# Optimization experiments

Hardware: AMD Instinct MI355X
Metric: run time of the kernel (lower is better)

## Reference

```python
import jax, jax.numpy as jnp
import numpy as np

N_NODE = 50000
N_EDGE = 800000
NODE_DIM, EDGE_DIM = 3, 4


def _relu(x):
    return jnp.maximum(x, 0)


def setup_inputs() -> dict:
    key = jax.random.key(0)
    ks = jax.random.split(key, 32)
    ki = iter(range(32))

    def w(shape):
        fan = shape[0]
        return (jax.random.normal(ks[next(ki)], shape, jnp.float32) / np.float32(np.sqrt(fan)))

    def b(n):
        return jnp.zeros((n,), jnp.float32)

    inp = {
        'nodes': jax.random.normal(ks[next(ki)], (N_NODE, NODE_DIM), jnp.float32),
        'edges': jax.random.normal(ks[next(ki)], (N_EDGE, EDGE_DIM), jnp.float32),
        'senders': jax.random.randint(ks[next(ki)], (N_EDGE,), 0, N_NODE, jnp.int32),
        'receivers': jax.random.randint(ks[next(ki)], (N_EDGE,), 0, N_NODE, jnp.int32),
        # psi1 encoder: [10 -> 256 -> 256 -> 128], relu after every layer (act_final=True)
        'mw0': w((NODE_DIM * 2 + EDGE_DIM, 256)), 'mb0': b(256),
        'mw1': w((256, 256)), 'mb1': b(256),
        'mw2': w((256, 128)), 'mb2': b(128),
        # psi2 attention: [128 -> 128 -> 128 -> 1], no final act
        'aw0': w((128, 128)), 'ab0': b(128),
        'aw1': w((128, 128)), 'ab1': b(128),
        'aw2': w((128, 1)), 'ab2': b(1),
        # psi3 value: [128 -> 256 -> 128], relu after every layer
        'vw0': w((128, 256)), 'vb0': b(256),
        'vw1': w((256, 128)), 'vb1': b(128),
        # psi4 decoder: [128 -> 256 -> 256 -> 1], no final act
        'uw0': w((128, 256)), 'ub0': b(256),
        'uw1': w((256, 256)), 'ub1': b(256),
        'uw2': w((256, 1)), 'ub2': b(1),
    }
    return inp


def reference(nodes, edges, senders, receivers,
              mw0, mb0, mw1, mb1, mw2, mb2,
              aw0, ab0, aw1, ab1, aw2, ab2,
              vw0, vb0, vw1, vb1,
              uw0, ub0, uw1, ub1, uw2, ub2):
    n_node = nodes.shape[0]
    # gather endpoint features and concat with edge features: (E, 2*node_dim+edge_dim)
    z = jnp.concatenate([nodes[senders], nodes[receivers], edges], axis=-1)
    # psi1 encoder (act_final=True)
    q = _relu(_relu(_relu(z @ mw0 + mb0) @ mw1 + mb1) @ mw2 + mb2)  # (E,128)
    # psi2 attention logits (no final act)
    w = (_relu(_relu(q @ aw0 + ab0) @ aw1 + ab1) @ aw2 + ab2)[:, 0]  # (E,)
    # segment softmax over receivers (matches torch scatter_reduce amax with -1e9 init)
    m = jax.ops.segment_max(w, receivers, num_segments=n_node)
    m = jnp.maximum(m, jnp.float32(-1e9))
    ex = jnp.exp(w - m[receivers])
    s = jax.ops.segment_sum(ex, receivers, num_segments=n_node)
    attn = ex / (s[receivers] + 1e-12)  # (E,)
    # psi3 value (act_final=True)
    v = _relu(_relu(q @ vw0 + vb0) @ vw1 + vb1)  # (E,128)
    # attention-weighted scatter-add aggregation to receiver nodes
    aggr = jax.ops.segment_sum(attn[:, None] * v, receivers, num_segments=n_node)  # (N,128)
    # psi4 decoder (no final act)
    out = _relu(_relu(aggr @ uw0 + ub0) @ uw1 + ub1) @ uw2 + ub2  # (N,1)
    return out
```

## Files before the change

kernel.cpp:

```cpp
#include <hip/hip_runtime.h>
#include <stdint.h>

#define NN_NODE 50000
#define NN_EDGE 800000

typedef _Float16 f16;
typedef _Float16 f16x2 __attribute__((ext_vector_type(2)));
typedef _Float16 f16x4 __attribute__((ext_vector_type(4)));
typedef _Float16 f16x8 __attribute__((ext_vector_type(8)));
typedef float f32x4 __attribute__((ext_vector_type(4)));

#define WT_MW0   0
#define WT_MW1   8192
#define WT_MW2   73728
#define WT_AW0   106496
#define WT_AW1   122880
#define WT_VW0   139264
#define WT_VW1   172032
#define WT_UW0   204800
#define WT_UW1   237568
#define WT_TOTAL 303104

#define V_OFF      606208ull
#define WL_OFF     205406208ull
#define CNT_OFF    208606208ull
#define BASE_OFF   208806208ull
#define AGGR_OFF   209006208ull

__device__ __forceinline__ int swz(int row, int col) {
    return row * 256 + ((((col >> 3) ^ (row & 7))) << 3) + (col & 7);
}

template<int K, int N, int NKN, int EPI>
__device__ __forceinline__ void mlayer(const f16* in, int inoff,
        const f16* __restrict__ wt, const float* __restrict__ bias,
        f16* out, int outoff,
        f16x8* bf0, const f16* __restrict__ wtn, f16x8* bfn,
        const float* __restrict__ aw2, float* lpart,
        f16* __restrict__ vout, const int* sposp, int tid)
{
    const int wave = tid >> 6;
    const int lane = tid & 63;
    const int l15  = lane & 15;
    const int quad = lane >> 4;
    constexpr int NKS = K >> 5;
    constexpr int NCT = N >> 4;
    constexpr int ITC = NCT / 4;

    f16x8 af[4][NKS];
#pragma unroll
    for (int ms = 0; ms < 4; ++ms)
#pragma unroll
        for (int ks = 0; ks < NKS; ++ks)
            af[ms][ks] = *(const f16x8*)(in + swz(ms * 16 + l15, inoff + ks * 32 + quad * 8));

    if constexpr (NKN > 0) {
        const f16* wrow = wtn + (size_t)(wave * 16 + l15) * (NKN * 32) + quad * 8;
#pragma unroll
        for (int ks = 0; ks < NKN; ++ks) bfn[ks] = *(const f16x8*)(wrow + ks * 32);
    }

    int   sposv[4];
    float preg[4];
    if constexpr (EPI == 2) {
#pragma unroll
        for (int ms = 0; ms < 4; ++ms) sposv[ms] = sposp[ms * 16 + l15];
    }
    if constexpr (EPI == 1) {
#pragma unroll
        for (int ms = 0; ms < 4; ++ms) preg[ms] = 0.f;
    }

    f16x8 bfl[2][NKS > 0 ? NKS : 1];
#pragma unroll
    for (int ks = 0; ks < NKS; ++ks) bfl[0][ks] = bf0[ks];

#pragma unroll
    for (int i = 0; i < ITC; ++i) {
        const int ct = wave + i * 4;
        if (i + 1 < ITC) {
            const f16* wrow = wt + (size_t)((ct + 4) * 16 + l15) * K + quad * 8;
#pragma unroll
            for (int ks = 0; ks < NKS; ++ks)
                bfl[(i + 1) & 1][ks] = *(const f16x8*)(wrow + ks * 32);
        }
        const int f0 = ct * 16 + quad * 4;
        const float4 bv = *(const float4*)(bias + f0);
        float4 awv;
        if constexpr (EPI == 1) awv = *(const float4*)(aw2 + f0);
#pragma unroll
        for (int ms = 0; ms < 4; ++ms) {
            f32x4 acc = {0.f, 0.f, 0.f, 0.f};
#pragma unroll
            for (int ks = 0; ks < NKS; ++ks)
                acc = __builtin_amdgcn_mfma_f32_16x16x32_f16(bfl[i & 1][ks], af[ms][ks], acc, 0, 0, 0);
            if constexpr (EPI == 0) {
                f16x4 o;
                o[0] = (f16)fmaxf(acc[0] + bv.x, 0.f);
                o[1] = (f16)fmaxf(acc[1] + bv.y, 0.f);
                o[2] = (f16)fmaxf(acc[2] + bv.z, 0.f);
                o[3] = (f16)fmaxf(acc[3] + bv.w, 0.f);
                *(f16x4*)(out + swz(ms * 16 + l15, outoff + f0)) = o;
            } else if constexpr (EPI == 1) {
                preg[ms] += fmaxf(acc[0] + bv.x, 0.f) * awv.x
                          + fmaxf(acc[1] + bv.y, 0.f) * awv.y
                          + fmaxf(acc[2] + bv.z, 0.f) * awv.z
                          + fmaxf(acc[3] + bv.w, 0.f) * awv.w;
            } else {
                f16x4 o;
                o[0] = (f16)fmaxf(acc[0] + bv.x, 0.f);
                o[1] = (f16)fmaxf(acc[1] + bv.y, 0.f);
                o[2] = (f16)fmaxf(acc[2] + bv.z, 0.f);
                o[3] = (f16)fmaxf(acc[3] + bv.w, 0.f);
                *(f16x4*)(vout + (size_t)sposv[ms] * 128 + f0) = o;
            }
        }
    }
    if constexpr (EPI == 1) {
#pragma unroll
        for (int ms = 0; ms < 4; ++ms) {
            float r = preg[ms];
            r += __shfl_xor(r, 16);
            r += __shfl_xor(r, 32);
            if (quad == 0) lpart[wave * 64 + ms * 16 + l15] = r;
        }
    }
}

template<int K, int N>
__device__ __forceinline__ void mfma_layer_basic(const f16* in, int inoff,
        const f16* __restrict__ wt, const float* __restrict__ bias,
        f16* out, int outoff, int tid)
{
    const int wave = tid >> 6;
    const int lane = tid & 63;
    const int l15  = lane & 15;
    const int quad = lane >> 4;
    constexpr int NCT = N >> 4;
    constexpr int NKS = K >> 5;
    f16x8 af[4][NKS];
#pragma unroll
    for (int ms = 0; ms < 4; ++ms)
#pragma unroll
        for (int ks = 0; ks < NKS; ++ks)
            af[ms][ks] = *(const f16x8*)(in + swz(ms * 16 + l15, inoff + ks * 32 + quad * 8));
#pragma unroll 1
    for (int ct = wave; ct < NCT; ct += 4) {
        f16x8 bf[NKS];
        const f16* wrow = wt + (size_t)(ct * 16 + l15) * K + quad * 8;
#pragma unroll
        for (int ks = 0; ks < NKS; ++ks) bf[ks] = *(const f16x8*)(wrow + ks * 32);
        const int f0 = ct * 16 + quad * 4;
        const float4 bv = *(const float4*)(bias + f0);
#pragma unroll
        for (int ms = 0; ms < 4; ++ms) {
            f32x4 acc = {0.f, 0.f, 0.f, 0.f};
#pragma unroll
            for (int ks = 0; ks < NKS; ++ks)
                acc = __builtin_amdgcn_mfma_f32_16x16x32_f16(bf[ks], af[ms][ks], acc, 0, 0, 0);
            f16x4 o;
            o[0] = (f16)fmaxf(acc[0] + bv.x, 0.f);
            o[1] = (f16)fmaxf(acc[1] + bv.y, 0.f);
            o[2] = (f16)fmaxf(acc[2] + bv.z, 0.f);
            o[3] = (f16)fmaxf(acc[3] + bv.w, 0.f);
            *(f16x4*)(out + swz(ms * 16 + l15, outoff + f0)) = o;
        }
    }
}

struct WSeg { const float* src; int K, N, Kpad, dstOff; };
struct WSegs { WSeg s[9]; };

__global__ void prep_kernel(WSegs segs, f16* __restrict__ wt) {
    int idx = blockIdx.x * 256 + threadIdx.x;
    if (idx >= WT_TOTAL) return;
    int off = idx;
#pragma unroll
    for (int i = 0; i < 9; ++i) {
        int sz = segs.s[i].N * segs.s[i].Kpad;
        if (off < sz) {
            int n = off / segs.s[i].Kpad;
            int k = off - n * segs.s[i].Kpad;
            f16 val = (f16)0.f;
            if (k < segs.s[i].K) val = (f16)segs.s[i].src[k * segs.s[i].N + n];
            wt[segs.s[i].dstOff + off] = val;
            return;
        }
        off -= sz;
    }
}

__global__ void hist_kernel(const int* __restrict__ receivers, int* __restrict__ cnt) {
    int e = blockIdx.x * 256 + threadIdx.x;
    atomicAdd(&cnt[receivers[e]], 1);
}

__global__ __launch_bounds__(1024) void scan_kernel(int* __restrict__ cnt, int* __restrict__ base) {
    __shared__ int psum[1024];
    const int tid = threadIdx.x;
    const int CH = (NN_NODE + 1023) / 1024;
    const int lo = tid * CH;
    const int hi = min(lo + CH, NN_NODE);
    int s = 0;
    for (int i = lo; i < hi; ++i) s += cnt[i];
    psum[tid] = s;
    __syncthreads();
    for (int d = 1; d < 1024; d <<= 1) {
        int v = (tid >= d) ? psum[tid - d] : 0;
        __syncthreads();
        psum[tid] += v;
        __syncthreads();
    }
    int run = psum[tid] - s;
    for (int i = lo; i < hi; ++i) {
        int c = cnt[i];
        base[i] = run;
        cnt[i] = run;
        run += c;
    }
}

__global__ __launch_bounds__(256, 2) void edge_kernel(
        const float* __restrict__ nodes, const float* __restrict__ edges,
        const int* __restrict__ senders, const int* __restrict__ receivers,
        const f16* __restrict__ wt,
        const float* __restrict__ mb0, const float* __restrict__ mb1, const float* __restrict__ mb2,
        const float* __restrict__ ab0, const float* __restrict__ ab1,
        const float* __restrict__ aw2, const float* __restrict__ ab2,
        const float* __restrict__ vb0, const float* __restrict__ vb1,
        f16* __restrict__ vout, float* __restrict__ wlog, int* __restrict__ cursor)
{
    __shared__ f16 ldsbuf[2 * 64 * 256];
    __shared__ int spos[64];
    __shared__ float lpart[256];
    f16* bufA = ldsbuf;
    f16* bufB = ldsbuf + 64 * 256;
    const int tid = threadIdx.x;
    const int e0 = blockIdx.x * 64;
    const int wave = tid >> 6;
    const int lane = tid & 63;
    const int l15  = lane & 15;
    const int quad = lane >> 4;

    f16x8 bfA[8], bfB[8];

    {
        const f16* wrow = wt + WT_MW0 + (size_t)(wave * 16 + l15) * 32 + quad * 8;
        bfA[0] = *(const f16x8*)wrow;
    }

    {
        const int e = tid & 63, c = tid >> 6;
        f16x8 zv = {(f16)0.f,(f16)0.f,(f16)0.f,(f16)0.f,(f16)0.f,(f16)0.f,(f16)0.f,(f16)0.f};
        if (c == 0) {
            int s = senders[e0 + e];
            int r = receivers[e0 + e];
            const float2 ev = *(const float2*)(edges + (size_t)(e0 + e) * 4);
            zv[0] = (f16)nodes[s * 3 + 0]; zv[1] = (f16)nodes[s * 3 + 1]; zv[2] = (f16)nodes[s * 3 + 2];
            zv[3] = (f16)nodes[r * 3 + 0]; zv[4] = (f16)nodes[r * 3 + 1]; zv[5] = (f16)nodes[r * 3 + 2];
            zv[6] = (f16)ev.x; zv[7] = (f16)ev.y;
        } else if (c == 1) {
            const float2 ev = *(const float2*)(edges + (size_t)(e0 + e) * 4 + 2);
            zv[0] = (f16)ev.x; zv[1] = (f16)ev.y;
        }
        *(f16x8*)(bufA + e * 256 + ((c ^ (e & 7)) << 3)) = zv;
    }
    __syncthreads();

    mlayer< 32, 256, 8, 0>(bufA, 0, wt + WT_MW0, mb0, bufB, 0, bfA, wt + WT_MW1, bfB,
                           nullptr, nullptr, nullptr, nullptr, tid);
    __syncthreads();
    mlayer<256, 256, 8, 0>(bufB, 0, wt + WT_MW1, mb1, bufA, 0, bfB, wt + WT_MW2, bfA,
                           nullptr, nullptr, nullptr, nullptr, tid);
    __syncthreads();
    mlayer<256, 128, 4, 0>(bufA, 0, wt + WT_MW2, mb2, bufB, 0, bfA, wt + WT_AW0, bfB,
                           nullptr, nullptr, nullptr, nullptr, tid);
    __syncthreads();
    mlayer<128, 128, 4, 0>(bufB, 0, wt + WT_AW0, ab0, bufA, 0, bfB, wt + WT_AW1, bfA,
                           nullptr, nullptr, nullptr, nullptr, tid);
    __syncthreads();
    mlayer<128, 128, 4, 1>(bufA, 0, wt + WT_AW1, ab1, nullptr, 0, bfA, wt + WT_VW0, bfB,
                           aw2, lpart, nullptr, nullptr, tid);
    __syncthreads();

    if (tid < 64) {
        float wv = lpart[tid] + lpart[64 + tid] + lpart[128 + tid] + lpart[192 + tid] + ab2[0];
        int r = receivers[e0 + tid];
        int pos = atomicAdd(&cursor[r], 1);
        spos[tid] = pos;
        wlog[pos] = wv;
    }
    mlayer<128, 256, 8, 0>(bufB, 0, wt + WT_VW0, vb0, bufA, 0, bfB, wt + WT_VW1, bfA,
                           nullptr, nullptr, nullptr, nullptr, tid);
    __syncthreads();
    mlayer<256, 128, 0, 2>(bufA, 0, wt + WT_VW1, vb1, nullptr, 0, bfA, nullptr, nullptr,
                           nullptr, nullptr, vout, spos, tid);
}

__global__ __launch_bounds__(256) void aggregate_kernel(
        const float* __restrict__ wlog, const f16* __restrict__ v,
        const int* __restrict__ base, float* __restrict__ aggr)
{
    const int tid = threadIdx.x;
    const int n = blockIdx.x * 4 + (tid >> 6);
    const int lane = tid & 63;
    const int st = base[n];
    const int en = (n == NN_NODE - 1) ? NN_EDGE : base[n + 1];

    float mx = -1e9f;
    for (int i = st + lane; i < en; i += 64) mx = fmaxf(mx, wlog[i]);
#pragma unroll
    for (int d = 1; d < 64; d <<= 1) mx = fmaxf(mx, __shfl_xor(mx, d));

    float sm = 0.f;
    for (int i = st + lane; i < en; i += 64) sm += __expf(wlog[i] - mx);
#pragma unroll
    for (int d = 1; d < 64; d <<= 1) sm += __shfl_xor(sm, d);
    const float inv = 1.f / (sm + 1e-12f);

    float acc0 = 0.f, acc1 = 0.f;
    const f16* vp = v + (size_t)st * 128 + lane * 2;
    for (int i = st; i < en; ++i, vp += 128) {
        float attn = __expf(wlog[i] - mx) * inv;
        f16x2 vv = *(const f16x2*)vp;
        acc0 += attn * (float)vv[0];
        acc1 += attn * (float)vv[1];
    }
    float2 o; o.x = acc0; o.y = acc1;
    *(float2*)(aggr + (size_t)n * 128 + lane * 2) = o;
}

__global__ __launch_bounds__(256, 2) void node_kernel(
        const float* __restrict__ aggr, const f16* __restrict__ wt,
        const float* __restrict__ ub0, const float* __restrict__ ub1,
        const float* __restrict__ uw2, const float* __restrict__ ub2,
        float* __restrict__ out)
{
    __shared__ f16 ldsbuf[2 * 64 * 256];
    f16* bufA = ldsbuf;
    f16* bufB = ldsbuf + 64 * 256;
    const int tid = threadIdx.x;
    const int n0 = blockIdx.x * 64;
    {
        int row = tid >> 2, j = tid & 3;
        int n = n0 + row;
        if (n < NN_NODE) {
            const float4* src = (const float4*)(aggr + (size_t)n * 128 + j * 32);
#pragma unroll
            for (int i = 0; i < 8; ++i) {
                float4 t4 = src[i];
                int c = j * 32 + i * 4;
                bufA[swz(row, c + 0)] = (f16)t4.x;
                bufA[swz(row, c + 1)] = (f16)t4.y;
                bufA[swz(row, c + 2)] = (f16)t4.z;
                bufA[swz(row, c + 3)] = (f16)t4.w;
            }
        } else {
#pragma unroll
            for (int i = 0; i < 32; ++i) bufA[swz(row, j * 32 + i)] = (f16)0.f;
        }
    }
    __syncthreads();
    mfma_layer_basic<128, 256>(bufA, 0, wt + WT_UW0, ub0, bufB, 0, tid); __syncthreads();
    mfma_layer_basic<256, 256>(bufB, 0, wt + WT_UW1, ub1, bufA, 0, tid); __syncthreads();
    {
        int e = tid >> 2, part = tid & 3;
        float sum = 0.f;
        for (int c = part * 64; c < part * 64 + 64; ++c)
            sum += (float)bufA[swz(e, c)] * uw2[c];
        sum += __shfl_down(sum, 2);
        sum += __shfl_down(sum, 1);
        int n = n0 + e;
        if (part == 0 && n < NN_NODE) out[n] = sum + ub2[0];
    }
}

extern "C" void kernel_launch(void* const* d_in, const int* in_sizes, int n_in,
                              void* d_out, int out_size, void* d_ws, size_t ws_size,
                              hipStream_t stream)
{
    const float* nodes     = (const float*)d_in[0];
    const float* edges     = (const float*)d_in[1];
    const int*   senders   = (const int*)d_in[2];
    const int*   receivers = (const int*)d_in[3];
    const float* mw0 = (const float*)d_in[4];  const float* mb0 = (const float*)d_in[5];
    const float* mw1 = (const float*)d_in[6];  const float* mb1 = (const float*)d_in[7];
    const float* mw2 = (const float*)d_in[8];  const float* mb2 = (const float*)d_in[9];
    const float* aw0 = (const float*)d_in[10]; const float* ab0 = (const float*)d_in[11];
    const float* aw1 = (const float*)d_in[12]; const float* ab1 = (const float*)d_in[13];
    const float* aw2 = (const float*)d_in[14]; const float* ab2 = (const float*)d_in[15];
    const float* vw0 = (const float*)d_in[16]; const float* vb0 = (const float*)d_in[17];
    const float* vw1 = (const float*)d_in[18]; const float* vb1 = (const float*)d_in[19];
    const float* uw0 = (const float*)d_in[20]; const float* ub0 = (const float*)d_in[21];
    const float* uw1 = (const float*)d_in[22]; const float* ub1 = (const float*)d_in[23];
    const float* uw2 = (const float*)d_in[24]; const float* ub2 = (const float*)d_in[25];

    char* ws = (char*)d_ws;
    f16*   wt   = (f16*)ws;
    f16*   vbuf = (f16*)(ws + V_OFF);
    float* wlog = (float*)(ws + WL_OFF);
    int*   cnt  = (int*)(ws + CNT_OFF);
    int*   base = (int*)(ws + BASE_OFF);
    float* aggr = (float*)(ws + AGGR_OFF);
    float* out  = (float*)d_out;

    hipMemsetAsync(cnt, 0, NN_NODE * sizeof(int), stream);

    WSegs segs = {{
        { mw0,  10, 256,  32, WT_MW0 },
        { mw1, 256, 256, 256, WT_MW1 },
        { mw2, 256, 128, 256, WT_MW2 },
        { aw0, 128, 128, 128, WT_AW0 },
        { aw1, 128, 128, 128, WT_AW1 },
        { vw0, 128, 256, 128, WT_VW0 },
        { vw1, 256, 128, 256, WT_VW1 },
        { uw0, 128, 256, 128, WT_UW0 },
        { uw1, 256, 256, 256, WT_UW1 },
    }};
    prep_kernel<<<(WT_TOTAL + 255) / 256, 256, 0, stream>>>(segs, wt);

    hist_kernel<<<NN_EDGE / 256, 256, 0, stream>>>(receivers, cnt);
    scan_kernel<<<1, 1024, 0, stream>>>(cnt, base);

    edge_kernel<<<NN_EDGE / 64, 256, 0, stream>>>(nodes, edges, senders, receivers, wt,
        mb0, mb1, mb2, ab0, ab1, aw2, ab2, vb0, vb1, vbuf, wlog, cnt);

    aggregate_kernel<<<NN_NODE / 4, 256, 0, stream>>>(wlog, vbuf, base, aggr);

    node_kernel<<<(NN_NODE + 63) / 64, 256, 0, stream>>>(aggr, wt, ub0, ub1, uw2, ub2, out);
}
```

Baseline: 995.7 us.

## Widen edge and node kernels to 8 waves and fuse decoder final dot

Edge and node kernels now launch 512 threads (8 waves), each wave owning fewer column tiles per layer, with launch bounds requesting 4 blocks per CU. The node kernel now uses the pipelined mlayer path with a fused final uw2 dot-product epilogue and vectorized packed f16 conversion when loading aggr. Output conversions use the packed cvt_pkrtz instruction, and the aggregate kernel clamps its segment bounds. More waves per block aim to hide latency and spread the MFMA work, but the 64 KB of LDS per block may limit how many blocks can actually reside on a CU.

```diff
diff --git a/kernel.cpp b/kernel.cpp
--- a/kernel.cpp
+++ b/kernel.cpp
@@ -31,12 +31,16 @@
     return row * 256 + ((((col >> 3) ^ (row & 7))) << 3) + (col & 7);
 }
 
-template<int K, int N, int NKN, int EPI>
+__device__ __forceinline__ f16x2 pk2(float a, float b) {
+    return __builtin_bit_cast(f16x2, __builtin_amdgcn_cvt_pkrtz(a, b));
+}
+
+template<int K, int N, int NKN, int EPI, int NW>
 __device__ __forceinline__ void mlayer(const f16* in, int inoff,
         const f16* __restrict__ wt, const float* __restrict__ bias,
         f16* out, int outoff,
         f16x8* bf0, const f16* __restrict__ wtn, f16x8* bfn,
-        const float* __restrict__ aw2, float* lpart,
+        const float* __restrict__ dvec, float* lpart,
         f16* __restrict__ vout, const int* sposp, int tid)
 {
     const int wave = tid >> 6;
@@ -45,7 +49,7 @@
     const int quad = lane >> 4;
     constexpr int NKS = K >> 5;
     constexpr int NCT = N >> 4;
-    constexpr int ITC = NCT / 4;
+    constexpr int ITC = NCT / NW;
 
     f16x8 af[4][NKS];
 #pragma unroll
@@ -77,9 +81,9 @@
 
 #pragma unroll
     for (int i = 0; i < ITC; ++i) {
-        const int ct = wave + i * 4;
+        const int ct = wave + i * NW;
         if (i + 1 < ITC) {
-            const f16* wrow = wt + (size_t)((ct + 4) * 16 + l15) * K + quad * 8;
+            const f16* wrow = wt + (size_t)((ct + NW) * 16 + l15) * K + quad * 8;
 #pragma unroll
             for (int ks = 0; ks < NKS; ++ks)
                 bfl[(i + 1) & 1][ks] = *(const f16x8*)(wrow + ks * 32);
@@ -87,32 +91,26 @@
         const int f0 = ct * 16 + quad * 4;
         const float4 bv = *(const float4*)(bias + f0);
         float4 awv;
-        if constexpr (EPI == 1) awv = *(const float4*)(aw2 + f0);
+        if constexpr (EPI == 1) awv = *(const float4*)(dvec + f0);
 #pragma unroll
         for (int ms = 0; ms < 4; ++ms) {
             f32x4 acc = {0.f, 0.f, 0.f, 0.f};
 #pragma unroll
             for (int ks = 0; ks < NKS; ++ks)
                 acc = __builtin_amdgcn_mfma_f32_16x16x32_f16(bfl[i & 1][ks], af[ms][ks], acc, 0, 0, 0);
-            if constexpr (EPI == 0) {
-                f16x4 o;
-                o[0] = (f16)fmaxf(acc[0] + bv.x, 0.f);
-                o[1] = (f16)fmaxf(acc[1] + bv.y, 0.f);
-                o[2] = (f16)fmaxf(acc[2] + bv.z, 0.f);
-                o[3] = (f16)fmaxf(acc[3] + bv.w, 0.f);
-                *(f16x4*)(out + swz(ms * 16 + l15, outoff + f0)) = o;
-            } else if constexpr (EPI == 1) {
+            if constexpr (EPI == 1) {
                 preg[ms] += fmaxf(acc[0] + bv.x, 0.f) * awv.x
                           + fmaxf(acc[1] + bv.y, 0.f) * awv.y
                           + fmaxf(acc[2] + bv.z, 0.f) * awv.z
                           + fmaxf(acc[3] + bv.w, 0.f) * awv.w;
             } else {
-                f16x4 o;
-                o[0] = (f16)fmaxf(acc[0] + bv.x, 0.f);
-                o[1] = (f16)fmaxf(acc[1] + bv.y, 0.f);
-                o[2] = (f16)fmaxf(acc[2] + bv.z, 0.f);
-                o[3] = (f16)fmaxf(acc[3] + bv.w, 0.f);
-                *(f16x4*)(vout + (size_t)sposv[ms] * 128 + f0) = o;
+                f16x2 lo = pk2(fmaxf(acc[0] + bv.x, 0.f), fmaxf(acc[1] + bv.y, 0.f));
+                f16x2 hi = pk2(fmaxf(acc[2] + bv.z, 0.f), fmaxf(acc[3] + bv.w, 0.f));
+                f16x4 o; o[0] = lo[0]; o[1] = lo[1]; o[2] = hi[0]; o[3] = hi[1];
+                if constexpr (EPI == 0)
+                    *(f16x4*)(out + swz(ms * 16 + l15, outoff + f0)) = o;
+                else
+                    *(f16x4*)(vout + (size_t)sposv[ms] * 128 + f0) = o;
             }
         }
     }
@@ -123,47 +121,6 @@
             r += __shfl_xor(r, 16);
             r += __shfl_xor(r, 32);
             if (quad == 0) lpart[wave * 64 + ms * 16 + l15] = r;
-        }
-    }
-}
-
-template<int K, int N>
-__device__ __forceinline__ void mfma_layer_basic(const f16* in, int inoff,
-        const f16* __restrict__ wt, const float* __restrict__ bias,
-        f16* out, int outoff, int tid)
-{
-    const int wave = tid >> 6;
-    const int lane = tid & 63;
-    const int l15  = lane & 15;
-    const int quad = lane >> 4;
-    constexpr int NCT = N >> 4;
-    constexpr int NKS = K >> 5;
-    f16x8 af[4][NKS];
-#pragma unroll
-    for (int ms = 0; ms < 4; ++ms)
-#pragma unroll
-        for (int ks = 0; ks < NKS; ++ks)
-            af[ms][ks] = *(const f16x8*)(in + swz(ms * 16 + l15, inoff + ks * 32 + quad * 8));
-#pragma unroll 1
-    for (int ct = wave; ct < NCT; ct += 4) {
-        f16x8 bf[NKS];
-        const f16* wrow = wt + (size_t)(ct * 16 + l15) * K + quad * 8;
-#pragma unroll
-        for (int ks = 0; ks < NKS; ++ks) bf[ks] = *(const f16x8*)(wrow + ks * 32);
-        const int f0 = ct * 16 + quad * 4;
-        const float4 bv = *(const float4*)(bias + f0);
-#pragma unroll
-        for (int ms = 0; ms < 4; ++ms) {
-            f32x4 acc = {0.f, 0.f, 0.f, 0.f};
-#pragma unroll
-            for (int ks = 0; ks < NKS; ++ks)
-                acc = __builtin_amdgcn_mfma_f32_16x16x32_f16(bf[ks], af[ms][ks], acc, 0, 0, 0);
-            f16x4 o;
-            o[0] = (f16)fmaxf(acc[0] + bv.x, 0.f);
-            o[1] = (f16)fmaxf(acc[1] + bv.y, 0.f);
-            o[2] = (f16)fmaxf(acc[2] + bv.z, 0.f);
-            o[3] = (f16)fmaxf(acc[3] + bv.w, 0.f);
-            *(f16x4*)(out + swz(ms * 16 + l15, outoff + f0)) = o;
         }
     }
 }
@@ -220,7 +177,7 @@
     }
 }
 
-__global__ __launch_bounds__(256, 2) void edge_kernel(
+__global__ __launch_bounds__(512, 4) void edge_kernel(
         const float* __restrict__ nodes, const float* __restrict__ edges,
         const int* __restrict__ senders, const int* __restrict__ receivers,
         const f16* __restrict__ wt,
@@ -232,7 +189,7 @@
 {
     __shared__ f16 ldsbuf[2 * 64 * 256];
     __shared__ int spos[64];
-    __shared__ float lpart[256];
+    __shared__ float lpart[512];
     f16* bufA = ldsbuf;
     f16* bufB = ldsbuf + 64 * 256;
     const int tid = threadIdx.x;
@@ -251,50 +208,54 @@
 
     {
         const int e = tid & 63, c = tid >> 6;
-        f16x8 zv = {(f16)0.f,(f16)0.f,(f16)0.f,(f16)0.f,(f16)0.f,(f16)0.f,(f16)0.f,(f16)0.f};
-        if (c == 0) {
-            int s = senders[e0 + e];
-            int r = receivers[e0 + e];
-            const float2 ev = *(const float2*)(edges + (size_t)(e0 + e) * 4);
-            zv[0] = (f16)nodes[s * 3 + 0]; zv[1] = (f16)nodes[s * 3 + 1]; zv[2] = (f16)nodes[s * 3 + 2];
-            zv[3] = (f16)nodes[r * 3 + 0]; zv[4] = (f16)nodes[r * 3 + 1]; zv[5] = (f16)nodes[r * 3 + 2];
-            zv[6] = (f16)ev.x; zv[7] = (f16)ev.y;
-        } else if (c == 1) {
-            const float2 ev = *(const float2*)(edges + (size_t)(e0 + e) * 4 + 2);
-            zv[0] = (f16)ev.x; zv[1] = (f16)ev.y;
-        }
-        *(f16x8*)(bufA + e * 256 + ((c ^ (e & 7)) << 3)) = zv;
-    }
-    __syncthreads();
-
-    mlayer< 32, 256, 8, 0>(bufA, 0, wt + WT_MW0, mb0, bufB, 0, bfA, wt + WT_MW1, bfB,
-                           nullptr, nullptr, nullptr, nullptr, tid);
-    __syncthreads();
-    mlayer<256, 256, 8, 0>(bufB, 0, wt + WT_MW1, mb1, bufA, 0, bfB, wt + WT_MW2, bfA,
-                           nullptr, nullptr, nullptr, nullptr, tid);
-    __syncthreads();
-    mlayer<256, 128, 4, 0>(bufA, 0, wt + WT_MW2, mb2, bufB, 0, bfA, wt + WT_AW0, bfB,
-                           nullptr, nullptr, nullptr, nullptr, tid);
-    __syncthreads();
-    mlayer<128, 128, 4, 0>(bufB, 0, wt + WT_AW0, ab0, bufA, 0, bfB, wt + WT_AW1, bfA,
-                           nullptr, nullptr, nullptr, nullptr, tid);
-    __syncthreads();
-    mlayer<128, 128, 4, 1>(bufA, 0, wt + WT_AW1, ab1, nullptr, 0, bfA, wt + WT_VW0, bfB,
-                           aw2, lpart, nullptr, nullptr, tid);
+        if (c < 4) {
+            f16x8 zv = {(f16)0.f,(f16)0.f,(f16)0.f,(f16)0.f,(f16)0.f,(f16)0.f,(f16)0.f,(f16)0.f};
+            if (c == 0) {
+                int s = senders[e0 + e];
+                int r = receivers[e0 + e];
+                const float2 ev = *(const float2*)(edges + (size_t)(e0 + e) * 4);
+                zv[0] = (f16)nodes[s * 3 + 0]; zv[1] = (f16)nodes[s * 3 + 1]; zv[2] = (f16)nodes[s * 3 + 2];
+                zv[3] = (f16)nodes[r * 3 + 0]; zv[4] = (f16)nodes[r * 3 + 1]; zv[5] = (f16)nodes[r * 3 + 2];
+                zv[6] = (f16)ev.x; zv[7] = (f16)ev.y;
+            } else if (c == 1) {
+                const float2 ev = *(const float2*)(edges + (size_t)(e0 + e) * 4 + 2);
+                zv[0] = (f16)ev.x; zv[1] = (f16)ev.y;
+            }
+            *(f16x8*)(bufA + e * 256 + ((c ^ (e & 7)) << 3)) = zv;
+        }
+    }
+    __syncthreads();
+
+    mlayer< 32, 256, 8, 0, 8>(bufA, 0, wt + WT_MW0, mb0, bufB, 0, bfA, wt + WT_MW1, bfB,
+                              nullptr, nullptr, nullptr, nullptr, tid);
+    __syncthreads();
+    mlayer<256, 256, 8, 0, 8>(bufB, 0, wt + WT_MW1, mb1, bufA, 0, bfB, wt + WT_MW2, bfA,
+                              nullptr, nullptr, nullptr, nullptr, tid);
+    __syncthreads();
+    mlayer<256, 128, 4, 0, 8>(bufA, 0, wt + WT_MW2, mb2, bufB, 0, bfA, wt + WT_AW0, bfB,
+                              nullptr, nullptr, nullptr, nullptr, tid);
+    __syncthreads();
+    mlayer<128, 128, 4, 0, 8>(bufB, 0, wt + WT_AW0, ab0, bufA, 0, bfB, wt + WT_AW1, bfA,
+                              nullptr, nullptr, nullptr, nullptr, tid);
+    __syncthreads();
+    mlayer<128, 128, 4, 1, 8>(bufA, 0, wt + WT_AW1, ab1, nullptr, 0, bfA, wt + WT_VW0, bfB,
+                              aw2, lpart, nullptr, nullptr, tid);
     __syncthreads();
 
     if (tid < 64) {
-        float wv = lpart[tid] + lpart[64 + tid] + lpart[128 + tid] + lpart[192 + tid] + ab2[0];
+        float wv = ab2[0];
+#pragma unroll
+        for (int w = 0; w < 8; ++w) wv += lpart[w * 64 + tid];
         int r = receivers[e0 + tid];
         int pos = atomicAdd(&cursor[r], 1);
         spos[tid] = pos;
         wlog[pos] = wv;
     }
-    mlayer<128, 256, 8, 0>(bufB, 0, wt + WT_VW0, vb0, bufA, 0, bfB, wt + WT_VW1, bfA,
-                           nullptr, nullptr, nullptr, nullptr, tid);
-    __syncthreads();
-    mlayer<256, 128, 0, 2>(bufA, 0, wt + WT_VW1, vb1, nullptr, 0, bfA, nullptr, nullptr,
-                           nullptr, nullptr, vout, spos, tid);
+    mlayer<128, 256, 8, 0, 8>(bufB, 0, wt + WT_VW0, vb0, bufA, 0, bfB, wt + WT_VW1, bfA,
+                              nullptr, nullptr, nullptr, nullptr, tid);
+    __syncthreads();
+    mlayer<256, 128, 0, 2, 8>(bufA, 0, wt + WT_VW1, vb1, nullptr, 0, bfA, nullptr, nullptr,
+                              nullptr, nullptr, vout, spos, tid);
 }
 
 __global__ __launch_bounds__(256) void aggregate_kernel(
@@ -304,8 +265,10 @@
     const int tid = threadIdx.x;
     const int n = blockIdx.x * 4 + (tid >> 6);
     const int lane = tid & 63;
-    const int st = base[n];
-    const int en = (n == NN_NODE - 1) ? NN_EDGE : base[n + 1];
+    int st = base[n];
+    int en = (n == NN_NODE - 1) ? NN_EDGE : base[n + 1];
+    st = max(0, min(st, NN_EDGE));
+    en = max(st, min(en, NN_EDGE));
 
     float mx = -1e9f;
     for (int i = st + lane; i < en; i += 64) mx = fmaxf(mx, wlog[i]);
@@ -330,48 +293,61 @@
     *(float2*)(aggr + (size_t)n * 128 + lane * 2) = o;
 }
 
-__global__ __launch_bounds__(256, 2) void node_kernel(
+__global__ __launch_bounds__(512, 4) void node_kernel(
         const float* __restrict__ aggr, const f16* __restrict__ wt,
         const float* __restrict__ ub0, const float* __restrict__ ub1,
         const float* __restrict__ uw2, const float* __restrict__ ub2,
         float* __restrict__ out)
 {
     __shared__ f16 ldsbuf[2 * 64 * 256];
+    __shared__ float lpart[512];
     f16* bufA = ldsbuf;
     f16* bufB = ldsbuf + 64 * 256;
     const int tid = threadIdx.x;
     const int n0 = blockIdx.x * 64;
+    const int wave = tid >> 6;
+    const int lane = tid & 63;
+    const int l15  = lane & 15;
+    const int quad = lane >> 4;
+
+    f16x8 bfA[8], bfB[8];
     {
-        int row = tid >> 2, j = tid & 3;
+        const f16* wrow = wt + WT_UW0 + (size_t)(wave * 16 + l15) * 128 + quad * 8;
+#pragma unroll
+        for (int ks = 0; ks < 4; ++ks) bfA[ks] = *(const f16x8*)(wrow + ks * 32);
+    }
+
+    {
+        int row = tid >> 3, j = tid & 7;
         int n = n0 + row;
+        f16x8 p0, p1;
         if (n < NN_NODE) {
-            const float4* src = (const float4*)(aggr + (size_t)n * 128 + j * 32);
-#pragma unroll
-            for (int i = 0; i < 8; ++i) {
-                float4 t4 = src[i];
-                int c = j * 32 + i * 4;
-                bufA[swz(row, c + 0)] = (f16)t4.x;
-                bufA[swz(row, c + 1)] = (f16)t4.y;
-                bufA[swz(row, c + 2)] = (f16)t4.z;
-                bufA[swz(row, c + 3)] = (f16)t4.w;
-            }
+            const float4* src = (const float4*)(aggr + (size_t)n * 128 + j * 16);
+            float4 a = src[0], b = src[1], c = src[2], d = src[3];
+            f16x2 q0 = pk2(a.x, a.y), q1 = pk2(a.z, a.w), q2 = pk2(b.x, b.y), q3 = pk2(b.z, b.w);
+            f16x2 q4 = pk2(c.x, c.y), q5 = pk2(c.z, c.w), q6 = pk2(d.x, d.y), q7 = pk2(d.z, d.w);
+            p0[0]=q0[0]; p0[1]=q0[1]; p0[2]=q1[0]; p0[3]=q1[1]; p0[4]=q2[0]; p0[5]=q2[1]; p0[6]=q3[0]; p0[7]=q3[1];
+            p1[0]=q4[0]; p1[1]=q4[1]; p1[2]=q5[0]; p1[3]=q5[1]; p1[4]=q6[0]; p1[5]=q6[1]; p1[6]=q7[0]; p1[7]=q7[1];
         } else {
-#pragma unroll
-            for (int i = 0; i < 32; ++i) bufA[swz(row, j * 32 + i)] = (f16)0.f;
-        }
-    }
-    __syncthreads();
-    mfma_layer_basic<128, 256>(bufA, 0, wt + WT_UW0, ub0, bufB, 0, tid); __syncthreads();
-    mfma_layer_basic<256, 256>(bufB, 0, wt + WT_UW1, ub1, bufA, 0, tid); __syncthreads();
-    {
-        int e = tid >> 2, part = tid & 3;
-        float sum = 0.f;
-        for (int c = part * 64; c < part * 64 + 64; ++c)
-            sum += (float)bufA[swz(e, c)] * uw2[c];
-        sum += __shfl_down(sum, 2);
-        sum += __shfl_down(sum, 1);
-        int n = n0 + e;
-        if (part == 0 && n < NN_NODE) out[n] = sum + ub2[0];
+            p0 = (f16x8)(f16)0.f; p1 = (f16x8)(f16)0.f;
+        }
+        *(f16x8*)(bufA + row * 256 + (((2 * j) ^ (row & 7)) << 3)) = p0;
+        *(f16x8*)(bufA + row * 256 + (((2 * j + 1) ^ (row & 7)) << 3)) = p1;
+    }
+    __syncthreads();
+
+    mlayer<128, 256, 8, 0, 8>(bufA, 0, wt + WT_UW0, ub0, bufB, 0, bfA, wt + WT_UW1, bfB,
+                              nullptr, nullptr, nullptr, nullptr, tid);
+    __syncthreads();
+    mlayer<256, 256, 0, 1, 8>(bufB, 0, wt + WT_UW1, ub1, nullptr, 0, bfB, nullptr, nullptr,
+                              uw2, lpart, nullptr, nullptr, tid);
+    __syncthreads();
+    if (tid < 64) {
+        float sum = ub2[0];
+#pragma unroll
+        for (int w = 0; w < 8; ++w) sum += lpart[w * 64 + tid];
+        int n = n0 + tid;
+        if (n < NN_NODE) out[n] = sum;
     }
 }
 
@@ -404,7 +380,7 @@
     float* aggr = (float*)(ws + AGGR_OFF);
     float* out  = (float*)d_out;
 
-    hipMemsetAsync(cnt, 0, NN_NODE * sizeof(int), stream);
+    (void)hipMemsetAsync(cnt, 0, NN_NODE * sizeof(int), stream);
 
     WSegs segs = {{
         { mw0,  10, 256,  32, WT_MW0 },
@@ -422,10 +398,10 @@
     hist_kernel<<<NN_EDGE / 256, 256, 0, stream>>>(receivers, cnt);
     scan_kernel<<<1, 1024, 0, stream>>>(cnt, base);
 
-    edge_kernel<<<NN_EDGE / 64, 256, 0, stream>>>(nodes, edges, senders, receivers, wt,
+    edge_kernel<<<NN_EDGE / 64, 512, 0, stream>>>(nodes, edges, senders, receivers, wt,
         mb0, mb1, mb2, ab0, ab1, aw2, ab2, vb0, vb1, vbuf, wlog, cnt);
 
     aggregate_kernel<<<NN_NODE / 4, 256, 0, stream>>>(wlog, vbuf, base, aggr);
 
-    node_kernel<<<(NN_NODE + 63) / 64, 256, 0, stream>>>(aggr, wt, ub0, ub1, uw2, ub2, out);
-}
+    node_kernel<<<(NN_NODE + 63) / 64, 512, 0, stream>>>(aggr, wt, ub0, ub1, uw2, ub2, out);
+}
```

New measurement: 1.188 ms. 19.3% more time.
